# Optimization experiments

Measured on AMD Instinct MI355X. Metric: run time of the kernel, lower is better.

## Reference

```python
import jax, jax.numpy as jnp
import numpy as np

B, N, C, OUT = 8, 2048, 128, 128

def setup_inputs() -> dict:
    key = jax.random.key(0)
    k1, k2, k3, k4, k5, k6 = jax.random.split(key, 6)
    x = jax.random.normal(k1, (B, N, C), dtype=jnp.float32)
    adj = jax.random.randint(k2, (B, N, N), 0, 2, dtype=jnp.int32)
    # fc: Linear(2*C, 1) + Sigmoid  (per-edge attention on concat(x_j, x_k))
    W_fc = jax.random.normal(k3, (2 * C, 1), dtype=jnp.float32) / np.sqrt(2 * C)
    b_fc = jax.random.normal(k4, (1,), dtype=jnp.float32) * 0.01
    # linear: Linear(C, OUT)
    W_lin = jax.random.normal(k5, (C, OUT), dtype=jnp.float32) / np.sqrt(C)
    b_lin = jax.random.normal(k6, (OUT,), dtype=jnp.float32) * 0.01
    return {"x": x, "adj": adj, "W_fc": W_fc, "b_fc": b_fc, "W_lin": W_lin, "b_lin": b_lin}

def reference(x, adj, W_fc, b_fc, W_lin, b_lin):
    # mode == 'global'
    # a_jk = sigmoid(W_fc . concat(x_j, x_k) + b_fc) where adj[j,k]==1, else 0.
    # Split the concat linear: score = (x_j . w1) + (x_k . w2) + b.
    Cdim = x.shape[-1]
    w1, w2 = W_fc[:Cdim, 0], W_fc[Cdim:, 0]
    sj = jnp.einsum('bnc,c->bn', x, w1)  # contribution of source node j
    sk = jnp.einsum('bnc,c->bn', x, w2)  # contribution of neighbor k
    scores = jax.nn.sigmoid(sj[:, :, None] + sk[:, None, :] + b_fc[0])  # [B,N,N]
    w = jnp.where(adj == 1, scores, jnp.float32(0))
    # row-normalize (divide each row by its sum)
    w = w / jnp.sum(w, axis=-1, keepdims=True)
    support = jnp.einsum('bjk,bkc->bjc', w, x)   # weighted aggregate
    return support @ W_lin + b_lin              # output projection
```

## Files before the change

kernel.cpp:

```cpp
#include <hip/hip_runtime.h>
#include <stdint.h>

#define BB 8
#define NN 2048
#define CC 128
#define OO 128

typedef __attribute__((ext_vector_type(8))) short bf16x8;
typedef __attribute__((ext_vector_type(4))) float f32x4;
typedef __attribute__((ext_vector_type(4))) int i32x4;
typedef __attribute__((ext_vector_type(4))) unsigned short u16x4;
typedef unsigned int u32;
typedef unsigned short u16;

__device__ __forceinline__ u16 f2bf(float f) {
    union { float f; u32 u; } v; v.f = f;
    u32 r = v.u + 0x7FFFu + ((v.u >> 16) & 1u);
    return (u16)(r >> 16);
}

__device__ __forceinline__ void gl_lds16(const u16* g, u16* l) {
    __builtin_amdgcn_global_load_lds(
        (__attribute__((address_space(1))) void*)(uintptr_t)g,
        (__attribute__((address_space(3))) void*)l, 16, 0, 0);
}

__global__ __launch_bounds__(256) void wt_kernel(
    const float* __restrict__ W_lin, u16* __restrict__ Wt)
{
    __shared__ float ws2[8][132];
    const int t = threadIdx.x, o0 = blockIdx.x * 8;
    f32x4 v = *(const f32x4*)(W_lin + (t >> 1) * OO + o0 + (t & 1) * 4);
    #pragma unroll
    for (int e = 0; e < 4; ++e) ws2[(t & 1) * 4 + e][t >> 1] = v[e];
    __syncthreads();
    const int oo = t >> 5, c0 = (t & 31) * 4;
    f32x4 u = *(const f32x4*)&ws2[oo][c0];
    u16x4 h;
    #pragma unroll
    for (int e = 0; e < 4; ++e) h[e] = f2bf(u[e]);
    *(u16x4*)(Wt + (size_t)(o0 + oo) * CC + c0) = h;
}

__global__ __launch_bounds__(256) void precompute_kernel(
    const float* __restrict__ x, const float* __restrict__ W_fc,
    const float* __restrict__ b_fc, const u16* __restrict__ Wt,
    float* __restrict__ sj, float* __restrict__ sk, u16* __restrict__ Yt)
{
    const int t = threadIdx.x, l = t & 63, w = t >> 6;
    const int sl = l & 15, g = l >> 4;
    const int b  = blockIdx.x >> 6;
    const int k0 = (blockIdx.x & 63) << 5;
    const int mt = w & 1, nb = (w >> 1) << 2;
    const int row = k0 + mt * 16 + sl;
    const float* xr = x + ((size_t)(b * NN + row) << 7);

    bf16x8 a[4];
    float p1 = 0.f, p2 = 0.f;
    #pragma unroll
    for (int ks = 0; ks < 4; ++ks) {
        f32x4 lo4 = *(const f32x4*)(xr + ks * 32 + g * 8);
        f32x4 hi4 = *(const f32x4*)(xr + ks * 32 + g * 8 + 4);
        f32x4 w1l = *(const f32x4*)(W_fc + ks * 32 + g * 8);
        f32x4 w1h = *(const f32x4*)(W_fc + ks * 32 + g * 8 + 4);
        f32x4 w2l = *(const f32x4*)(W_fc + CC + ks * 32 + g * 8);
        f32x4 w2h = *(const f32x4*)(W_fc + CC + ks * 32 + g * 8 + 4);
        bf16x8 av;
        #pragma unroll
        for (int e = 0; e < 4; ++e) {
            p1 += lo4[e] * w1l[e] + hi4[e] * w1h[e];
            p2 += lo4[e] * w2l[e] + hi4[e] * w2h[e];
            av[e]     = (short)f2bf(lo4[e]);
            av[e + 4] = (short)f2bf(hi4[e]);
        }
        a[ks] = av;
    }
    p1 += __shfl_xor(p1, 16); p1 += __shfl_xor(p1, 32);
    p2 += __shfl_xor(p2, 16); p2 += __shfl_xor(p2, 32);
    if (w < 2 && g == 0) {
        sj[b * NN + row] = p1 + b_fc[0];
        sk[b * NN + row] = p2;
    }

    f32x4 acc[4];
    #pragma unroll
    for (int i = 0; i < 4; ++i) acc[i] = (f32x4){0.f, 0.f, 0.f, 0.f};
    #pragma unroll
    for (int i = 0; i < 4; ++i) {
        const u16* wp = Wt + (size_t)((nb + i) * 16 + sl) * CC;
        #pragma unroll
        for (int ks = 0; ks < 4; ++ks) {
            bf16x8 bv = *(const bf16x8*)(wp + ks * 32 + g * 8);
            acc[i] = __builtin_amdgcn_mfma_f32_16x16x32_bf16(a[ks], bv, acc[i], 0, 0, 0);
        }
    }
    #pragma unroll
    for (int i = 0; i < 4; ++i) {
        const int o = (nb + i) * 16 + sl;
        u16x4 h;
        #pragma unroll
        for (int e = 0; e < 4; ++e) h[e] = f2bf(acc[i][e]);
        *(u16x4*)(Yt + (size_t)(b * OO + o) * NN + k0 + mt * 16 + g * 4) = h;
    }
}

__global__ __launch_bounds__(256, 2) void graphconv_main(
    const int* __restrict__ adj, const float* __restrict__ sj,
    const float* __restrict__ sk, const u16* __restrict__ Yt,
    const float* __restrict__ b_lin, float* __restrict__ out)
{
    __shared__ __align__(16) u16 ybuf[2][16384];
    __shared__ __align__(16) u16 pbuf[4096];
    __shared__ float Sld[32];

    const int t  = threadIdx.x;
    const int l  = t & 63, w = t >> 6;
    const int sw = l & 15, kg = l >> 4;
    const int lo = l & 31, hi = l >> 5;
    const int b  = blockIdx.x & 7;
    const int j0 = (blockIdx.x >> 3) << 5;

    const int* arow[4];
    float sjr[4];
    #pragma unroll
    for (int q = 0; q < 4; ++q) {
        const int R = j0 + w * 8 + 2 * q + hi;
        arow[q] = adj + ((size_t)b * NN + R) * NN + lo * 4;
        sjr[q]  = sj[b * NN + R];
    }
    const float* skp = sk + b * NN + lo * 4;

    u32 yoff[8];
    #pragma unroll
    for (int i = 0; i < 8; ++i) {
        int u  = (w * 8 + i) * 64 + l;
        int o  = u >> 4;
        int kc = (u & 15) ^ (o & 15);
        yoff[i] = (u32)(b * OO + o) * NN + kc * 8;
    }

    f32x4 acc[2][2];
    #pragma unroll
    for (int js = 0; js < 2; ++js)
        #pragma unroll
        for (int os = 0; os < 2; ++os) acc[js][os] = (f32x4){0.f, 0.f, 0.f, 0.f};
    float psum[4] = {0.f, 0.f, 0.f, 0.f};

    #pragma unroll
    for (int i = 0; i < 8; ++i)
        gl_lds16(Yt + yoff[i], &ybuf[0][(w * 8 + i) * 512]);
    i32x4 a_cur[4], a_n1[4];
    f32x4 s_cur, s_n1;
    #pragma unroll
    for (int q = 0; q < 4; ++q) a_cur[q] = *(const i32x4*)(arow[q]);
    s_cur = *(const f32x4*)(skp);
    #pragma unroll
    for (int q = 0; q < 4; ++q) a_n1[q] = *(const i32x4*)(arow[q] + 128);
    s_n1 = *(const f32x4*)(skp + 128);

    for (int kt = 0; kt < 16; ++kt) {
        const int cur = kt & 1;
        const int kt1 = (kt < 15) ? kt + 1 : 15;
        const int kt2 = (kt < 14) ? kt + 2 : 15;
        #pragma unroll
        for (int i = 0; i < 8; ++i)
            gl_lds16(Yt + yoff[i] + (kt1 << 7), &ybuf[cur ^ 1][(w * 8 + i) * 512]);
        i32x4 a_n2[4]; f32x4 s_n2;
        #pragma unroll
        for (int q = 0; q < 4; ++q) a_n2[q] = *(const i32x4*)(arow[q] + kt2 * 128);
        s_n2 = *(const f32x4*)(skp + kt2 * 128);

        u16x4 hq[4];
        #pragma unroll
        for (int q = 0; q < 4; ++q) {
            #pragma unroll
            for (int e = 0; e < 4; ++e) {
                float z  = sjr[q] + s_cur[e];
                float sg = __builtin_amdgcn_rcpf(1.0f + __expf(-z));
                float pv = a_cur[q][e] ? sg : 0.0f;
                psum[q] += pv;
                hq[q][e] = f2bf(pv);
            }
        }
        {
            const int kc = lo >> 1, hh = lo & 1;
            #pragma unroll
            for (int q = 0; q < 4; ++q) {
                const int R = w * 8 + 2 * q + hi;
                const int u = R * 16 + (kc ^ (R & 15));
                *(u16x4*)&pbuf[u * 8 + hh * 4] = hq[q];
            }
        }

        asm volatile("s_waitcnt vmcnt(18)" ::: "memory");
        asm volatile("s_waitcnt lgkmcnt(0)" ::: "memory");
        __builtin_amdgcn_s_barrier();
        asm volatile("" ::: "memory");

        #pragma unroll
        for (int kk = 0; kk < 4; ++kk) {
            const int kc = kk * 4 + kg;
            bf16x8 af[2], bfr[2];
            #pragma unroll
            for (int js = 0; js < 2; ++js)
                af[js] = *(const bf16x8*)&pbuf[((js * 16 + sw) * 16 + (kc ^ sw)) * 8];
            #pragma unroll
            for (int os = 0; os < 2; ++os) {
                int o = w * 32 + os * 16 + sw;
                bfr[os] = *(const bf16x8*)&ybuf[cur][(o * 16 + (kc ^ sw)) * 8];
            }
            #pragma unroll
            for (int js = 0; js < 2; ++js)
                #pragma unroll
                for (int os = 0; os < 2; ++os)
                    acc[js][os] = __builtin_amdgcn_mfma_f32_16x16x32_bf16(
                        af[js], bfr[os], acc[js][os], 0, 0, 0);
        }

        asm volatile("" ::: "memory");
        __builtin_amdgcn_s_barrier();
        asm volatile("" ::: "memory");

        #pragma unroll
        for (int q = 0; q < 4; ++q) a_cur[q] = a_n1[q];
        s_cur = s_n1;
        #pragma unroll
        for (int q = 0; q < 4; ++q) a_n1[q] = a_n2[q];
        s_n1 = s_n2;
    }

    #pragma unroll
    for (int q = 0; q < 4; ++q) {
        float s = psum[q];
        s += __shfl_xor(s, 1); s += __shfl_xor(s, 2); s += __shfl_xor(s, 4);
        s += __shfl_xor(s, 8); s += __shfl_xor(s, 16);
        if (lo == 0) Sld[w * 8 + 2 * q + hi] = s;
    }
    __syncthreads();

    #pragma unroll
    for (int js = 0; js < 2; ++js) {
        float rinv[4];
        #pragma unroll
        for (int i = 0; i < 4; ++i) rinv[i] = 1.0f / Sld[js * 16 + kg * 4 + i];
        #pragma unroll
        for (int os = 0; os < 2; ++os) {
            const int col = w * 32 + os * 16 + sw;
            const float bl = b_lin[col];
            #pragma unroll
            for (int i = 0; i < 4; ++i) {
                size_t row = (size_t)(b * NN + j0 + js * 16 + kg * 4 + i);
                out[row * OO + col] = acc[js][os][i] * rinv[i] + bl;
            }
        }
    }
}

extern "C" void kernel_launch(void* const* d_in, const int* in_sizes, int n_in,
                              void* d_out, int out_size, void* d_ws, size_t ws_size,
                              hipStream_t stream) {
    const float* x     = (const float*)d_in[0];
    const int*   adj   = (const int*)d_in[1];
    const float* W_fc  = (const float*)d_in[2];
    const float* b_fc  = (const float*)d_in[3];
    const float* W_lin = (const float*)d_in[4];
    const float* b_lin = (const float*)d_in[5];
    float* out = (float*)d_out;

    u16*   Yt = (u16*)d_ws;
    float* sj = (float*)((char*)d_ws + (size_t)BB * OO * NN * sizeof(u16));
    float* sk = sj + BB * NN;
    u16*   Wt = (u16*)(sk + BB * NN);

    wt_kernel<<<16, 256, 0, stream>>>(W_lin, Wt);
    precompute_kernel<<<512, 256, 0, stream>>>(x, W_fc, b_fc, Wt, sj, sk, Yt);
    graphconv_main<<<512, 256, 0, stream>>>(adj, sj, sk, Yt, b_lin, out);
}
```

Baseline: 50.77 us.

## Bit-pack adjacency in a pre-pass and read bitmasks in main kernel

Adds a pre-pass kernel that reads the int32 adjacency matrix once and packs it into 64-bit ballot masks in workspace. The main graph-convolution kernel then loads one 32-bit word per lane per tile instead of four int32 values per row, and extracts each mask bit with a shift. The aim is to strip the large adjacency stream out of the compute-heavy main kernel so its loads are small and easier to hide. The full adjacency read still happens, now in a separate bandwidth-bound launch, and there is an extra kernel launch plus a small write and read-back of the packed masks.

Result: slower. 67.03 us (+32.0%).

```diff
diff --git a/kernel.cpp b/kernel.cpp
--- a/kernel.cpp
+++ b/kernel.cpp
@@ -12,6 +12,7 @@
 typedef __attribute__((ext_vector_type(4))) unsigned short u16x4;
 typedef unsigned int u32;
 typedef unsigned short u16;
+typedef unsigned long long u64;
 
 __device__ __forceinline__ u16 f2bf(float f) {
     union { float f; u32 u; } v; v.f = f;
@@ -23,6 +24,21 @@
     __builtin_amdgcn_global_load_lds(
         (__attribute__((address_space(1))) void*)(uintptr_t)g,
         (__attribute__((address_space(3))) void*)l, 16, 0, 0);
+}
+
+__global__ __launch_bounds__(256) void bits_kernel(
+    const int* __restrict__ adj, u64* __restrict__ bits)
+{
+    const int l = threadIdx.x & 63;
+    const u32 wglob = (blockIdx.x * 256 + threadIdx.x) >> 6;
+    const size_t base = (size_t)wglob * 64;
+    #pragma unroll 8
+    for (int s = 0; s < 64; ++s) {
+        size_t g = base + s;
+        int v = adj[g * 64 + l];
+        u64 m = __ballot(v != 0);
+        if (l == 0) bits[g] = m;
+    }
 }
 
 __global__ __launch_bounds__(256) void wt_kernel(
@@ -105,7 +121,7 @@
 }
 
 __global__ __launch_bounds__(256, 2) void graphconv_main(
-    const int* __restrict__ adj, const float* __restrict__ sj,
+    const u32* __restrict__ bits32, const float* __restrict__ sj,
     const float* __restrict__ sk, const u16* __restrict__ Yt,
     const float* __restrict__ b_lin, float* __restrict__ out)
 {
@@ -120,14 +136,15 @@
     const int b  = blockIdx.x & 7;
     const int j0 = (blockIdx.x >> 3) << 5;
 
-    const int* arow[4];
+    const u32* brow[4];
     float sjr[4];
     #pragma unroll
     for (int q = 0; q < 4; ++q) {
         const int R = j0 + w * 8 + 2 * q + hi;
-        arow[q] = adj + ((size_t)b * NN + R) * NN + lo * 4;
+        brow[q] = bits32 + ((size_t)b * NN + R) * 64 + (lo >> 3);
         sjr[q]  = sj[b * NN + R];
     }
+    const int nsh = (lo & 7) * 4;
     const float* skp = sk + b * NN + lo * 4;
 
     u32 yoff[8];
@@ -149,13 +166,13 @@
     #pragma unroll
     for (int i = 0; i < 8; ++i)
         gl_lds16(Yt + yoff[i], &ybuf[0][(w * 8 + i) * 512]);
-    i32x4 a_cur[4], a_n1[4];
+    u32 a_cur[4], a_n1[4];
     f32x4 s_cur, s_n1;
     #pragma unroll
-    for (int q = 0; q < 4; ++q) a_cur[q] = *(const i32x4*)(arow[q]);
+    for (int q = 0; q < 4; ++q) a_cur[q] = brow[q][0];
     s_cur = *(const f32x4*)(skp);
     #pragma unroll
-    for (int q = 0; q < 4; ++q) a_n1[q] = *(const i32x4*)(arow[q] + 128);
+    for (int q = 0; q < 4; ++q) a_n1[q] = brow[q][4];
     s_n1 = *(const f32x4*)(skp + 128);
 
     for (int kt = 0; kt < 16; ++kt) {
@@ -165,9 +182,9 @@
         #pragma unroll
         for (int i = 0; i < 8; ++i)
             gl_lds16(Yt + yoff[i] + (kt1 << 7), &ybuf[cur ^ 1][(w * 8 + i) * 512]);
-        i32x4 a_n2[4]; f32x4 s_n2;
-        #pragma unroll
-        for (int q = 0; q < 4; ++q) a_n2[q] = *(const i32x4*)(arow[q] + kt2 * 128);
+        u32 a_n2[4]; f32x4 s_n2;
+        #pragma unroll
+        for (int q = 0; q < 4; ++q) a_n2[q] = brow[q][kt2 * 4];
         s_n2 = *(const f32x4*)(skp + kt2 * 128);
 
         u16x4 hq[4];
@@ -177,7 +194,7 @@
             for (int e = 0; e < 4; ++e) {
                 float z  = sjr[q] + s_cur[e];
                 float sg = __builtin_amdgcn_rcpf(1.0f + __expf(-z));
-                float pv = a_cur[q][e] ? sg : 0.0f;
+                float pv = ((a_cur[q] >> (nsh + e)) & 1u) ? sg : 0.0f;
                 psum[q] += pv;
                 hq[q][e] = f2bf(pv);
             }
@@ -271,8 +288,10 @@
     float* sj = (float*)((char*)d_ws + (size_t)BB * OO * NN * sizeof(u16));
     float* sk = sj + BB * NN;
     u16*   Wt = (u16*)(sk + BB * NN);
-
+    u64*   bits = (u64*)((char*)d_ws + 4ull * 1024 * 1024 + 256 * 1024);
+
+    bits_kernel<<<2048, 256, 0, stream>>>(adj, bits);
     wt_kernel<<<16, 256, 0, stream>>>(W_lin, Wt);
     precompute_kernel<<<512, 256, 0, stream>>>(x, W_fc, b_fc, Wt, sj, sk, Yt);
-    graphconv_main<<<512, 256, 0, stream>>>(adj, sj, sk, Yt, b_lin, out);
-}
+    graphconv_main<<<512, 256, 0, stream>>>((const u32*)bits, sj, sk, Yt, b_lin, out);
+}
```
